# Optimization experiments

Hardware: AMD Instinct MI355X
Metric: run time of the kernel (lower is better)

## Reference

```python
import jax, jax.numpy as jnp
import numpy as np

N_NODES = 100000
N_EDGES = 3200000
D_FEAT = 256
GC_HID = 20      # CVAEEncoder.hidden_dim default
DEC_HID = 40     # CVAEDecoder.hidden_dim default
Z_DIM = 32
EXPR_DIM = 256
SIGMA_BOUND = 0.0001


def setup_inputs() -> dict:
    key = jax.random.key(0)
    ks = jax.random.split(key, 16)
    inp = {
        "nodes": jax.random.normal(ks[0], (N_NODES, D_FEAT), dtype=jnp.float32),
        "senders": jax.random.randint(ks[1], (N_EDGES,), 0, N_NODES, dtype=jnp.int32),
        "receivers": jax.random.randint(ks[2], (N_EDGES,), 0, N_NODES, dtype=jnp.int32),
        "eps": jax.random.normal(ks[3], (N_NODES, Z_DIM), dtype=jnp.float32),
    }
    def dense(k, fan_in, fan_out):
        # flax default: lecun_normal kernel, zero bias
        w = jax.random.normal(k, (fan_in, fan_out), dtype=jnp.float32) / np.sqrt(fan_in)
        return w, jnp.zeros((fan_out,), jnp.float32)
    inp["W_gc1"], inp["b_gc1"] = dense(ks[4], D_FEAT, GC_HID)
    inp["W_gc2"], inp["b_gc2"] = dense(ks[5], GC_HID, GC_HID)
    inp["W_mu"], inp["b_mu"] = dense(ks[6], GC_HID + D_FEAT, Z_DIM)
    inp["W_ls"], inp["b_ls"] = dense(ks[7], GC_HID + D_FEAT, Z_DIM)
    inp["W_d1"], inp["b_d1"] = dense(ks[8], Z_DIM, DEC_HID)
    inp["W_d2"], inp["b_d2"] = dense(ks[9], DEC_HID, EXPR_DIM)
    return inp


def _gcn_layer(h, senders, receivers, W, b):
    # jraph.GraphConvolution: update_node_fn = softmax(relu(Dense(x))),
    # then symmetric-normalized segment_sum aggregation (no self edges).
    h = jax.nn.softmax(jax.nn.relu(h @ W + b), axis=-1)  # [N, GC_HID]
    ones = jnp.ones(senders.shape, h.dtype)
    deg_s = jax.ops.segment_sum(ones, senders, N_NODES)
    deg_r = jax.ops.segment_sum(ones, receivers, N_NODES)
    h = h * jax.lax.rsqrt(jnp.maximum(deg_s, 1.0))[:, None]
    h = jax.ops.segment_sum(h[senders], receivers, N_NODES)  # irregular gather+scatter
    h = h * jax.lax.rsqrt(jnp.maximum(deg_r, 1.0))[:, None]
    return h


def reference(nodes, senders, receivers, eps,
              W_gc1, b_gc1, W_gc2, b_gc2,
              W_mu, b_mu, W_ls, b_ls,
              W_d1, b_d1, W_d2, b_d2):
    # Encoder: 2 GC layers
    h = _gcn_layer(nodes, senders, receivers, W_gc1, b_gc1)
    h = _gcn_layer(h, senders, receivers, W_gc2, b_gc2)
    h = jnp.concatenate([h, nodes], axis=-1)  # [N, GC_HID + D_FEAT]
    mu = h @ W_mu + b_mu
    logsig2 = h @ W_ls + b_ls
    # Reparameterization
    sigma = SIGMA_BOUND + jnp.exp(0.5 * logsig2)
    z = mu + sigma * eps
    # Decoder MLP (nlayers=2 -> one hidden relu layer)
    d = jax.nn.relu(z @ W_d1 + b_d1)
    Xsample = d @ W_d2 + b_d2
    return Xsample, mu, logsig2
```

## Files before the change

kernel.cpp:

```cpp
#include <hip/hip_runtime.h>
#include <math.h>

#define N_NODES 100000
#define N_EDGES 3200000
#define D_FEAT 256
#define GC_HID 20
#define DEC_HID 40
#define Z_DIM 32

#define EPB 2048
#define NBLK 1563
#define SB 392
#define SBSH 8
#define S2CAP 12288


__device__ inline unsigned short f2bf(float f) {
    unsigned u = __float_as_uint(f);
    return (unsigned short)((u + 0x7FFFu + ((u >> 16) & 1u)) >> 16);
}
__device__ inline float bf2f(unsigned short h) {
    return __uint_as_float((unsigned)h << 16);
}

__global__ __launch_bounds__(96) void k_wpack(const float* __restrict__ W1,
                                              const float* __restrict__ Wmu,
                                              const float* __restrict__ Wls,
                                              float* __restrict__ Wp) {
    int k = blockIdx.x, j = threadIdx.x;
    float v = 0.0f;
    if (j < 20) v = W1[k * GC_HID + j];
    else if (j >= 24 && j < 56) v = Wmu[(GC_HID + k) * Z_DIM + (j - 24)];
    else if (j >= 56 && j < 88) v = Wls[(GC_HID + k) * Z_DIM + (j - 56)];
    Wp[k * 96 + j] = v;
}

__global__ __launch_bounds__(512) void k_sort(const int* __restrict__ snd,
                                              const int* __restrict__ rcv,
                                              unsigned* __restrict__ rec_r,
                                              unsigned char* __restrict__ rec_s,
                                              unsigned short* __restrict__ srow_r,
                                              unsigned short* __restrict__ srow_s) {
    __shared__ int es[EPB], er[EPB];
    __shared__ unsigned scan[SB + 1];
    __shared__ unsigned cur[SB];
    __shared__ unsigned sorted[EPB];
    __shared__ unsigned char sorteds[EPB];
    int b = blockIdx.x, t = threadIdx.x;
    int base = b * EPB;
    int cnt = min(EPB, N_EDGES - base);
    for (int i = t; i < cnt; i += 512) { es[i] = snd[base + i]; er[i] = rcv[base + i]; }

    for (int i = t; i < SB + 1; i += 512) scan[i] = 0u;
    __syncthreads();
    for (int i = t; i < cnt; i += 512) atomicAdd(&scan[(er[i] >> SBSH) + 1], 1u);
    __syncthreads();
    for (int off = 1; off < SB + 1; off <<= 1) {
        unsigned v = (t >= off && t < SB + 1) ? scan[t - off] : 0u;
        __syncthreads();
        if (t < SB + 1) scan[t] += v;
        __syncthreads();
    }
    for (int i = t; i < SB + 1; i += 512) srow_r[(size_t)b * (SB + 1) + i] = (unsigned short)scan[i];
    if (t < SB) cur[t] = scan[t];
    __syncthreads();
    for (int i = t; i < cnt; i += 512) {
        int r = er[i];
        unsigned pos = atomicAdd(&cur[r >> SBSH], 1u);
        sorted[pos] = ((unsigned)(r & 255) << 17) | (unsigned)es[i];
    }
    __syncthreads();
    for (int i = t; i < cnt; i += 512) rec_r[(size_t)base + i] = sorted[i];
    __syncthreads();

    for (int i = t; i < SB + 1; i += 512) scan[i] = 0u;
    __syncthreads();
    for (int i = t; i < cnt; i += 512) atomicAdd(&scan[(es[i] >> SBSH) + 1], 1u);
    __syncthreads();
    for (int off = 1; off < SB + 1; off <<= 1) {
        unsigned v = (t >= off && t < SB + 1) ? scan[t - off] : 0u;
        __syncthreads();
        if (t < SB + 1) scan[t] += v;
        __syncthreads();
    }
    for (int i = t; i < SB + 1; i += 512) srow_s[(size_t)b * (SB + 1) + i] = (unsigned short)scan[i];
    if (t < SB) cur[t] = scan[t];
    __syncthreads();
    for (int i = t; i < cnt; i += 512) {
        int s = es[i];
        unsigned pos = atomicAdd(&cur[s >> SBSH], 1u);
        sorteds[pos] = (unsigned char)(s & 255);
    }
    __syncthreads();
    for (int i = t; i < cnt; i += 512) rec_s[(size_t)base + i] = sorteds[i];
}

__global__ __launch_bounds__(512) void k_degs(const unsigned char* __restrict__ rec_s,
                                              const unsigned short* __restrict__ srow_s,
                                              float* __restrict__ rs_s) {
    __shared__ unsigned h[256];
    int s = blockIdx.x, t = threadIdx.x;
    if (t < 256) h[t] = 0u;
    __syncthreads();
    for (int k = t; k < NBLK; k += 512) {
        const unsigned short* row = srow_s + (size_t)k * (SB + 1);
        unsigned st = row[s], en = row[s + 1];
        const unsigned char* rp = rec_s + (size_t)k * EPB;
        for (unsigned i = st; i < en; ++i) atomicAdd(&h[rp[i]], 1u);
    }
    __syncthreads();
    if (t < 256) {
        int n = (s << SBSH) + t;
        if (n < N_NODES) rs_s[n] = rsqrtf(fmaxf((float)h[t], 1.0f));
    }
}

__global__ __launch_bounds__(256) void k_scanB(const unsigned short* __restrict__ srow_r,
                                               unsigned* __restrict__ pref_t,
                                               unsigned* __restrict__ gtot) {
    __shared__ unsigned buf[256];
    int s = blockIdx.x, t = threadIdx.x;
    unsigned run = 0;
    for (int k0 = 0; k0 < NBLK; k0 += 256) {
        int k = k0 + t;
        unsigned v = 0;
        if (k < NBLK) {
            const unsigned short* row = srow_r + (size_t)k * (SB + 1);
            v = (unsigned)row[s + 1] - (unsigned)row[s];
        }
        buf[t] = v;
        __syncthreads();
        for (int off = 1; off < 256; off <<= 1) {
            unsigned x = (t >= off) ? buf[t - off] : 0u;
            __syncthreads();
            buf[t] += x;
            __syncthreads();
        }
        if (k < NBLK) pref_t[(size_t)s * NBLK + k] = run + (buf[t] - v);
        unsigned tot = buf[255];
        __syncthreads();
        run += tot;
    }
    if (t == 0) gtot[s] = run;
}

__global__ __launch_bounds__(512) void k_scanG(const unsigned* __restrict__ gtot,
                                               unsigned* __restrict__ gbase) {
    __shared__ unsigned buf[SB];
    int t = threadIdx.x;
    if (t < SB) buf[t] = gtot[t];
    __syncthreads();
    for (int off = 1; off < SB; off <<= 1) {
        unsigned x = (t >= off && t < SB) ? buf[t - off] : 0u;
        __syncthreads();
        if (t < SB) buf[t] += x;
        __syncthreads();
    }
    if (t < SB) gbase[t + 1] = buf[t];
    if (t == 0) gbase[0] = 0u;
}

__global__ __launch_bounds__(256) void k_gscat(const unsigned* __restrict__ rec_r,
                                               const unsigned short* __restrict__ srow_r,
                                               const unsigned* __restrict__ pref_t,
                                               const unsigned* __restrict__ gbase,
                                               unsigned* __restrict__ grec) {
    __shared__ unsigned recs[EPB];
    __shared__ unsigned short srow[SB + 1];
    int b = blockIdx.x, t = threadIdx.x;
    int base = b * EPB;
    int cnt = min(EPB, N_EDGES - base);
    for (int i = t; i < cnt; i += 256) recs[i] = rec_r[(size_t)base + i];
    for (int i = t; i < SB + 1; i += 256) srow[i] = srow_r[(size_t)b * (SB + 1) + i];
    __syncthreads();
    for (int s = t; s < SB; s += 256) {
        unsigned lo = srow[s], hi = srow[s + 1];
        if (lo == hi) continue;
        unsigned dst = gbase[s] + pref_t[(size_t)s * NBLK + b];
        for (unsigned i = lo; i < hi; ++i) grec[dst + (i - lo)] = recs[i];
    }
}

__global__ __launch_bounds__(256) void k_sort2(unsigned* __restrict__ grec,
                                               const unsigned* __restrict__ gbase,
                                               unsigned* __restrict__ row_ptr) {
    __shared__ unsigned recs[S2CAP];
    __shared__ unsigned hist[256];
    __shared__ unsigned scan[256];
    __shared__ unsigned cur[256];
    int s = blockIdx.x, t = threadIdx.x;
    unsigned lo = gbase[s], hi = gbase[s + 1];
    unsigned cnt = min(hi - lo, (unsigned)S2CAP);
    for (unsigned i = t; i < cnt; i += 256) recs[i] = grec[lo + i];
    hist[t] = 0u;
    __syncthreads();
    for (unsigned i = t; i < cnt; i += 256) atomicAdd(&hist[recs[i] >> 17], 1u);
    __syncthreads();
    unsigned v = hist[t];
    scan[t] = v;
    __syncthreads();
    for (int off = 1; off < 256; off <<= 1) {
        unsigned x = (t >= off) ? scan[t - off] : 0u;
        __syncthreads();
        scan[t] += x;
        __syncthreads();
    }
    unsigned excl = scan[t] - v;
    {
        int n = (s << SBSH) + t;
        if (n <= N_NODES) row_ptr[n] = lo + excl;
    }
    cur[t] = excl;
    __syncthreads();
    for (unsigned i = t; i < cnt; i += 256) {
        unsigned rec = recs[i];
        unsigned pos = atomicAdd(&cur[rec >> 17], 1u);
        grec[lo + pos] = rec & 0x1FFFFu;
    }
}

__global__ __launch_bounds__(320) void k_gather(const unsigned* __restrict__ row_ptr,
                                                const unsigned* __restrict__ grec,
                                                const float* __restrict__ src,
                                                float* __restrict__ dst) {
    int gid = blockIdx.x * 320 + threadIdx.x;
    int node = gid / 5, q = gid % 5;
    if (node >= N_NODES) return;
    unsigned lo = row_ptr[node], hi = row_ptr[node + 1];
    float4 a0 = make_float4(0.f, 0.f, 0.f, 0.f);
    float4 a1 = make_float4(0.f, 0.f, 0.f, 0.f);
    float4 a2 = make_float4(0.f, 0.f, 0.f, 0.f);
    float4 a3 = make_float4(0.f, 0.f, 0.f, 0.f);
    unsigned e = lo;
    for (; e + 4 <= hi; e += 4) {
        unsigned s0 = grec[e], s1 = grec[e + 1], s2 = grec[e + 2], s3 = grec[e + 3];
        float4 v0 = ((const float4*)src)[s0 * 5 + q];
        float4 v1 = ((const float4*)src)[s1 * 5 + q];
        float4 v2 = ((const float4*)src)[s2 * 5 + q];
        float4 v3 = ((const float4*)src)[s3 * 5 + q];
        a0.x += v0.x; a0.y += v0.y; a0.z += v0.z; a0.w += v0.w;
        a1.x += v1.x; a1.y += v1.y; a1.z += v1.z; a1.w += v1.w;
        a2.x += v2.x; a2.y += v2.y; a2.z += v2.z; a2.w += v2.w;
        a3.x += v3.x; a3.y += v3.y; a3.z += v3.z; a3.w += v3.w;
    }
    for (; e < hi; ++e) {
        unsigned s0 = grec[e];
        float4 v0 = ((const float4*)src)[s0 * 5 + q];
        a0.x += v0.x; a0.y += v0.y; a0.z += v0.z; a0.w += v0.w;
    }
    a0.x += a1.x + a2.x + a3.x;
    a0.y += a1.y + a2.y + a3.y;
    a0.z += a1.z + a2.z + a3.z;
    a0.w += a1.w + a2.w + a3.w;
    float sc = rsqrtf(fmaxf((float)(hi - lo), 1.0f));
    a0.x *= sc; a0.y *= sc; a0.z *= sc; a0.w *= sc;
    ((float4*)dst)[node * 5 + q] = a0;
}

__global__ __launch_bounds__(320) void k_gg1(const unsigned* __restrict__ row_ptr,
                                             const unsigned* __restrict__ grec,
                                             const float* __restrict__ src,
                                             const float* __restrict__ W2,
                                             const float* __restrict__ b2,
                                             const float* __restrict__ rs_s,
                                             float* __restrict__ h2_pre) {
    __shared__ float h1[64 * 21];
    __shared__ float Wsh[GC_HID * GC_HID];
    __shared__ float bsh[GC_HID];
    int t = threadIdx.x;
    if (t < GC_HID * GC_HID) Wsh[t] = W2[t];
    if (t >= 400 && t < 400 + GC_HID) bsh[t - 400] = b2[t - 400];
    int nl = t / 5, q = t % 5;
    int node = blockIdx.x * 64 + nl;
    bool live = (node < N_NODES);
    unsigned lo = 0, hi = 0;
    if (live) { lo = row_ptr[node]; hi = row_ptr[node + 1]; }
    float4 a0 = make_float4(0.f, 0.f, 0.f, 0.f);
    float4 a1 = make_float4(0.f, 0.f, 0.f, 0.f);
    float4 a2 = make_float4(0.f, 0.f, 0.f, 0.f);
    float4 a3 = make_float4(0.f, 0.f, 0.f, 0.f);
    unsigned e = lo;
    for (; e + 4 <= hi; e += 4) {
        unsigned s0 = grec[e], s1 = grec[e + 1], s2 = grec[e + 2], s3 = grec[e + 3];
        float4 v0 = ((const float4*)src)[s0 * 5 + q];
        float4 v1 = ((const float4*)src)[s1 * 5 + q];
        float4 v2 = ((const float4*)src)[s2 * 5 + q];
        float4 v3 = ((const float4*)src)[s3 * 5 + q];
        a0.x += v0.x; a0.y += v0.y; a0.z += v0.z; a0.w += v0.w;
        a1.x += v1.x; a1.y += v1.y; a1.z += v1.z; a1.w += v1.w;
        a2.x += v2.x; a2.y += v2.y; a2.z += v2.z; a2.w += v2.w;
        a3.x += v3.x; a3.y += v3.y; a3.z += v3.z; a3.w += v3.w;
    }
    for (; e < hi; ++e) {
        unsigned s0 = grec[e];
        float4 v0 = ((const float4*)src)[s0 * 5 + q];
        a0.x += v0.x; a0.y += v0.y; a0.z += v0.z; a0.w += v0.w;
    }
    a0.x += a1.x + a2.x + a3.x;
    a0.y += a1.y + a2.y + a3.y;
    a0.z += a1.z + a2.z + a3.z;
    a0.w += a1.w + a2.w + a3.w;
    if (live) {
        float sc = rsqrtf(fmaxf((float)(hi - lo), 1.0f));
        float* row = &h1[nl * 21 + q * 4];
        row[0] = a0.x * sc; row[1] = a0.y * sc;
        row[2] = a0.z * sc; row[3] = a0.w * sc;
    }
    __syncthreads();
    if (t < 64) {
        int nn = blockIdx.x * 64 + t;
        if (nn < N_NODES) {
            float hv[GC_HID];
#pragma unroll
            for (int i = 0; i < GC_HID; ++i) hv[i] = h1[t * 21 + i];
            float o[GC_HID];
#pragma unroll
            for (int j = 0; j < GC_HID; ++j) o[j] = bsh[j];
#pragma unroll
            for (int i = 0; i < GC_HID; ++i) {
                float x = hv[i];
#pragma unroll
                for (int j = 0; j < GC_HID; ++j) o[j] = fmaf(x, Wsh[i * GC_HID + j], o[j]);
            }
            float mx = -1e30f;
#pragma unroll
            for (int j = 0; j < GC_HID; ++j) { o[j] = fmaxf(o[j], 0.0f); mx = fmaxf(mx, o[j]); }
            float s = 0.0f;
#pragma unroll
            for (int j = 0; j < GC_HID; ++j) { o[j] = __expf(o[j] - mx); s += o[j]; }
            float inv = rs_s[nn] / s;
#pragma unroll
            for (int j = 0; j < GC_HID; ++j) o[j] *= inv;
            float4* op = (float4*)&h2_pre[(size_t)nn * GC_HID];
            op[0] = make_float4(o[0],  o[1],  o[2],  o[3]);
            op[1] = make_float4(o[4],  o[5],  o[6],  o[7]);
            op[2] = make_float4(o[8],  o[9],  o[10], o[11]);
            op[3] = make_float4(o[12], o[13], o[14], o[15]);
            op[4] = make_float4(o[16], o[17], o[18], o[19]);
        }
    }
}

__global__ __launch_bounds__(256) void k_gc1f(const float* __restrict__ nodes,
                                              const float* __restrict__ Wp,
                                              const float* __restrict__ b1,
                                              const float* __restrict__ rs_s,
                                              float* __restrict__ h_pre,
                                              unsigned short* __restrict__ pml) {
    __shared__ float tile[2][64 * 33];
    float* gb = &tile[0][0];
    int t = threadIdx.x;
    int g = __builtin_amdgcn_readfirstlane(t >> 6);
    int lane = t & 63;
    int n0 = blockIdx.x * 64;
    int node = n0 + lane;

    {
        int idx = t;
#pragma unroll
        for (int r = 0; r < 2; ++r, idx += 256) {
            int rr = idx >> 3, c4 = idx & 7;
            int gn = n0 + rr;
            float4 v = (gn < N_NODES)
                ? ((const float4*)nodes)[(size_t)gn * 64 + c4]
                : make_float4(0.f, 0.f, 0.f, 0.f);
            float* dst = &tile[0][rr * 33 + c4 * 4];
            dst[0] = v.x; dst[1] = v.y; dst[2] = v.z; dst[3] = v.w;
        }
    }
    __syncthreads();

    float acc[24];
#pragma unroll
    for (int j = 0; j < 24; ++j) acc[j] = 0.0f;

    for (int c = 0; c < 8; ++c) {
        float4 p0, p1;
        if (c < 7) {
            int idx = t, rr = idx >> 3, c4 = idx & 7, gn = n0 + rr;
            p0 = (gn < N_NODES)
                ? ((const float4*)nodes)[(size_t)gn * 64 + (c + 1) * 8 + c4]
                : make_float4(0.f, 0.f, 0.f, 0.f);
            idx = t + 256; rr = idx >> 3; c4 = idx & 7; gn = n0 + rr;
            p1 = (gn < N_NODES)
                ? ((const float4*)nodes)[(size_t)gn * 64 + (c + 1) * 8 + c4]
                : make_float4(0.f, 0.f, 0.f, 0.f);
        }
        const float* trow  = &tile[c & 1][lane * 33];
        const float* wbase = Wp + (size_t)(c * 32) * 96 + g * 24;
#pragma unroll 4
        for (int kk = 0; kk < 32; ++kk) {
            float x = trow[kk];
            const float* wr = wbase + kk * 96;
#pragma unroll
            for (int j = 0; j < 24; ++j) acc[j] = fmaf(x, wr[j], acc[j]);
        }
        if (c < 7) {
            int idx = t, rr = idx >> 3, c4 = idx & 7;
            float* dst = &tile[(c + 1) & 1][rr * 33 + c4 * 4];
            dst[0] = p0.x; dst[1] = p0.y; dst[2] = p0.z; dst[3] = p0.w;
            idx = t + 256; rr = idx >> 3; c4 = idx & 7;
            dst = &tile[(c + 1) & 1][rr * 33 + c4 * 4];
            dst[0] = p1.x; dst[1] = p1.y; dst[2] = p1.z; dst[3] = p1.w;
        }
        __syncthreads();
    }

    if (node < N_NODES) {
        if (g == 0) {
#pragma unroll
            for (int j = 0; j < GC_HID; ++j) gb[lane * 21 + j] = acc[j] + b1[j];
        } else {
            int base = (g - 1) * 24;
            unsigned short* pp = pml + (size_t)node * 64 + base;
            uint4 q0, q1, q2;
            q0.x = (unsigned)f2bf(acc[0]) | ((unsigned)f2bf(acc[1]) << 16);
            q0.y = (unsigned)f2bf(acc[2]) | ((unsigned)f2bf(acc[3]) << 16);
            q0.z = (unsigned)f2bf(acc[4]) | ((unsigned)f2bf(acc[5]) << 16);
            q0.w = (unsigned)f2bf(acc[6]) | ((unsigned)f2bf(acc[7]) << 16);
            q1.x = (unsigned)f2bf(acc[8]) | ((unsigned)f2bf(acc[9]) << 16);
            q1.y = (unsigned)f2bf(acc[10]) | ((unsigned)f2bf(acc[11]) << 16);
            q1.z = (unsigned)f2bf(acc[12]) | ((unsigned)f2bf(acc[13]) << 16);
            q1.w = (unsigned)f2bf(acc[14]) | ((unsigned)f2bf(acc[15]) << 16);
            q2.x = (unsigned)f2bf(acc[16]) | ((unsigned)f2bf(acc[17]) << 16);
            q2.y = (unsigned)f2bf(acc[18]) | ((unsigned)f2bf(acc[19]) << 16);
            q2.z = (unsigned)f2bf(acc[20]) | ((unsigned)f2bf(acc[21]) << 16);
            q2.w = (unsigned)f2bf(acc[22]) | ((unsigned)f2bf(acc[23]) << 16);
            ((uint4*)pp)[0] = q0;
            ((uint4*)pp)[1] = q1;
            if (g != 3) ((uint4*)pp)[2] = q2;
        }
    }
    __syncthreads();
    if (t < 64) {
        int nn = n0 + t;
        if (nn < N_NODES) {
            float v[GC_HID];
            float mx = -1e30f;
#pragma unroll
            for (int j = 0; j < GC_HID; ++j) {
                v[j] = fmaxf(gb[t * 21 + j], 0.0f);
                mx = fmaxf(mx, v[j]);
            }
            float s = 0.0f;
#pragma unroll
            for (int j = 0; j < GC_HID; ++j) {
                v[j] = __expf(v[j] - mx);
                s += v[j];
            }
            float inv = rs_s[nn] / s;
#pragma unroll
            for (int j = 0; j < GC_HID; ++j) v[j] *= inv;
            float4* o = (float4*)&h_pre[(size_t)nn * GC_HID];
            o[0] = make_float4(v[0],  v[1],  v[2],  v[3]);
            o[1] = make_float4(v[4],  v[5],  v[6],  v[7]);
            o[2] = make_float4(v[8],  v[9],  v[10], v[11]);
            o[3] = make_float4(v[12], v[13], v[14], v[15]);
            o[4] = make_float4(v[16], v[17], v[18], v[19]);
        }
    }
}

__global__ __launch_bounds__(256) void k_enc2(const float* __restrict__ h2in,
                                              const unsigned short* __restrict__ pml,
                                              const float* __restrict__ Wmu,
                                              const float* __restrict__ bmu,
                                              const float* __restrict__ Wls,
                                              const float* __restrict__ bls,
                                              float* __restrict__ mu_out,
                                              float* __restrict__ ls_out) {
    int t = threadIdx.x;
    int wave = t >> 6, lane = t & 63;
    int og = __builtin_amdgcn_readfirstlane(wave | ((int)blockIdx.y << 2));
    int half = og >> 2;
    int co = (og & 3) << 3;
    int node = blockIdx.x * 64 + lane;
    if (node >= N_NODES) return;
    const float* W  = half ? Wls : Wmu;
    const float* bb = half ? bls : bmu;
    float* out      = half ? ls_out : mu_out;

    uint4 p = *(const uint4*)(pml + (size_t)node * 64 + half * 32 + co);
    float acc[8];
    acc[0] = bf2f((unsigned short)(p.x & 0xFFFFu));
    acc[1] = bf2f((unsigned short)(p.x >> 16));
    acc[2] = bf2f((unsigned short)(p.y & 0xFFFFu));
    acc[3] = bf2f((unsigned short)(p.y >> 16));
    acc[4] = bf2f((unsigned short)(p.z & 0xFFFFu));
    acc[5] = bf2f((unsigned short)(p.z >> 16));
    acc[6] = bf2f((unsigned short)(p.w & 0xFFFFu));
    acc[7] = bf2f((unsigned short)(p.w >> 16));
#pragma unroll
    for (int j = 0; j < 8; ++j) acc[j] += bb[co + j];

    const float4* hp = (const float4*)(h2in + (size_t)node * GC_HID);
#pragma unroll
    for (int v = 0; v < 5; ++v) {
        float4 hh = hp[v];
#pragma unroll
        for (int c = 0; c < 4; ++c) {
            float x = (c == 0) ? hh.x : (c == 1) ? hh.y : (c == 2) ? hh.z : hh.w;
            const float* wr = W + (v * 4 + c) * Z_DIM + co;
#pragma unroll
            for (int j = 0; j < 8; ++j) acc[j] = fmaf(x, wr[j], acc[j]);
        }
    }
    float4* op = (float4*)(out + (size_t)node * Z_DIM + co);
    op[0] = make_float4(acc[0], acc[1], acc[2], acc[3]);
    op[1] = make_float4(acc[4], acc[5], acc[6], acc[7]);
}

__global__ __launch_bounds__(256) void k_decd(const float* __restrict__ mu,
                                              const float* __restrict__ ls,
                                              const float* __restrict__ eps,
                                              const float* __restrict__ Wd1,
                                              const float* __restrict__ bd1,
                                              float* __restrict__ dbuf) {
    int node = blockIdx.x * 256 + threadIdx.x;
    if (node >= N_NODES) return;
    float d[DEC_HID];
#pragma unroll
    for (int j = 0; j < DEC_HID; ++j) d[j] = bd1[j];
    const float4* mp = (const float4*)(mu + (size_t)node * Z_DIM);
    const float4* lp = (const float4*)(ls + (size_t)node * Z_DIM);
    const float4* ep = (const float4*)(eps + (size_t)node * Z_DIM);
#pragma unroll
    for (int v = 0; v < Z_DIM / 4; ++v) {
        float4 m = mp[v], l = lp[v], e = ep[v];
        float4 zz;
        zz.x = m.x + (1e-4f + __expf(0.5f * l.x)) * e.x;
        zz.y = m.y + (1e-4f + __expf(0.5f * l.y)) * e.y;
        zz.z = m.z + (1e-4f + __expf(0.5f * l.z)) * e.z;
        zz.w = m.w + (1e-4f + __expf(0.5f * l.w)) * e.w;
#pragma unroll
        for (int c = 0; c < 4; ++c) {
            float x = (c == 0) ? zz.x : (c == 1) ? zz.y : (c == 2) ? zz.z : zz.w;
            const float* wr = Wd1 + (v * 4 + c) * DEC_HID;
#pragma unroll
            for (int j = 0; j < DEC_HID; ++j) d[j] = fmaf(x, wr[j], d[j]);
        }
    }
    float4* op = (float4*)(dbuf + (size_t)node * DEC_HID);
#pragma unroll
    for (int v = 0; v < DEC_HID / 4; ++v)
        op[v] = make_float4(fmaxf(d[4*v], 0.f), fmaxf(d[4*v+1], 0.f),
                            fmaxf(d[4*v+2], 0.f), fmaxf(d[4*v+3], 0.f));
}

__global__ __launch_bounds__(256) void k_decx(const float* __restrict__ dbuf,
                                              const float* __restrict__ Wd2,
                                              const float* __restrict__ bd2,
                                              float* __restrict__ X) {
    int lane = threadIdx.x & 63;
    int wv   = threadIdx.x >> 6;
    int ch   = __builtin_amdgcn_readfirstlane(((blockIdx.x & 1) << 2) | wv);
    int node = (blockIdx.x >> 1) * 64 + lane;
    if (node >= N_NODES) return;
    int co = ch << 5;
    float o[32];
#pragma unroll
    for (int j = 0; j < 32; ++j) o[j] = bd2[co + j];
    const float4* dp = (const float4*)(dbuf + (size_t)node * DEC_HID);
#pragma unroll
    for (int v = 0; v < DEC_HID / 4; ++v) {
        float4 dd = dp[v];
#pragma unroll
        for (int c = 0; c < 4; ++c) {
            float x = (c == 0) ? dd.x : (c == 1) ? dd.y : (c == 2) ? dd.z : dd.w;
            const float* wr = Wd2 + (v * 4 + c) * D_FEAT + co;
#pragma unroll
            for (int j = 0; j < 32; ++j) o[j] = fmaf(x, wr[j], o[j]);
        }
    }
    float4* xp = (float4*)(X + (size_t)node * D_FEAT + co);
#pragma unroll
    for (int v = 0; v < 8; ++v)
        xp[v] = make_float4(o[4*v], o[4*v+1], o[4*v+2], o[4*v+3]);
}

extern "C" void kernel_launch(void* const* d_in, const int* in_sizes, int n_in,
                              void* d_out, int out_size, void* d_ws, size_t ws_size,
                              hipStream_t stream) {
    const float* nodes = (const float*)d_in[0];
    const int*   snd   = (const int*)d_in[1];
    const int*   rcv   = (const int*)d_in[2];
    const float* eps   = (const float*)d_in[3];
    const float* W1    = (const float*)d_in[4];
    const float* b1    = (const float*)d_in[5];
    const float* W2    = (const float*)d_in[6];
    const float* b2    = (const float*)d_in[7];
    const float* Wmu   = (const float*)d_in[8];
    const float* bmu   = (const float*)d_in[9];
    const float* Wls   = (const float*)d_in[10];
    const float* bls   = (const float*)d_in[11];
    const float* Wd1   = (const float*)d_in[12];
    const float* bd1   = (const float*)d_in[13];
    const float* Wd2   = (const float*)d_in[14];
    const float* bd2   = (const float*)d_in[15];

    char* ws = (char*)d_ws;
    float*          h_pre    = (float*)(ws);
    float*          agg      = (float*)(ws + 8000000);
    float*          dbuf     = (float*)(ws);
    unsigned*       grec     = (unsigned*)(ws + 16000000);
    unsigned*       rec_r    = (unsigned*)(ws + 28804096);
    unsigned short* pml      = (unsigned short*)(ws + 28804096);
    unsigned short* srow_r   = (unsigned short*)(ws + 41608192);
    unsigned*       pref_t   = (unsigned*)(ws + 42836720);
    unsigned*       row_ptr  = (unsigned*)(ws + 45287504);
    unsigned*       gtot     = (unsigned*)(ws + 45687508);
    unsigned*       gbase    = (unsigned*)(ws + 45689076);
    float*          rs_s     = (float*)(ws + 45690648);
    unsigned char*  rec_s    = (unsigned char*)(ws + 46090648);
    unsigned short* srow_s   = (unsigned short*)(ws + 49291672);
    float*          Wpack    = (float*)(ws + 50520192);

    float* X      = (float*)d_out;
    float* mu_out = X + (size_t)N_NODES * D_FEAT;
    float* ls_out = mu_out + (size_t)N_NODES * Z_DIM;

    k_wpack<<<256, 96, 0, stream>>>(W1, Wmu, Wls, Wpack);
    k_sort<<<NBLK, 512, 0, stream>>>(snd, rcv, rec_r, rec_s, srow_r, srow_s);
    k_degs<<<SB, 512, 0, stream>>>(rec_s, srow_s, rs_s);
    k_scanB<<<SB, 256, 0, stream>>>(srow_r, pref_t, gtot);
    k_scanG<<<1, 512, 0, stream>>>(gtot, gbase);
    k_gscat<<<NBLK, 256, 0, stream>>>(rec_r, srow_r, pref_t, gbase, grec);
    k_sort2<<<SB, 256, 0, stream>>>(grec, gbase, row_ptr);

    k_gc1f<<<1563, 256, 0, stream>>>(nodes, Wpack, b1, rs_s, h_pre, pml);
    k_gg1<<<1563, 320, 0, stream>>>(row_ptr, grec, h_pre, W2, b2, rs_s, agg);
    k_gather<<<1563, 320, 0, stream>>>(row_ptr, grec, agg, h_pre);

    k_enc2<<<dim3(1563, 2), 256, 0, stream>>>(h_pre, pml, Wmu, bmu, Wls, bls,
                                              mu_out, ls_out);
    k_decd<<<391, 256, 0, stream>>>(mu_out, ls_out, eps, Wd1, bd1, dbuf);
    k_decx<<<3126, 256, 0, stream>>>(dbuf, Wd2, bd2, X);
}
```

Measured before the change: 417.8 us.

## Fuse second gather with mu/logsig projection and merge decoder kernels

Merges the second-layer neighbor gather with the mu/logsig projection. The aggregated hidden vector goes to shared memory and is consumed straight away, so no h2 round-trip through global memory is needed. Also fuses the two decoder kernels into one, keeping the 40-wide hidden activation in shared memory instead of writing and re-reading dbuf. This removes launches and intermediate global traffic. In exchange, the gather phase leaves 192 of 512 threads idle, and the fused kernels have larger blocks, which may lower occupancy.

```diff
diff --git a/kernel.cpp b/kernel.cpp
--- a/kernel.cpp
+++ b/kernel.cpp
@@ -217,44 +217,6 @@
         unsigned pos = atomicAdd(&cur[rec >> 17], 1u);
         grec[lo + pos] = rec & 0x1FFFFu;
     }
-}
-
-__global__ __launch_bounds__(320) void k_gather(const unsigned* __restrict__ row_ptr,
-                                                const unsigned* __restrict__ grec,
-                                                const float* __restrict__ src,
-                                                float* __restrict__ dst) {
-    int gid = blockIdx.x * 320 + threadIdx.x;
-    int node = gid / 5, q = gid % 5;
-    if (node >= N_NODES) return;
-    unsigned lo = row_ptr[node], hi = row_ptr[node + 1];
-    float4 a0 = make_float4(0.f, 0.f, 0.f, 0.f);
-    float4 a1 = make_float4(0.f, 0.f, 0.f, 0.f);
-    float4 a2 = make_float4(0.f, 0.f, 0.f, 0.f);
-    float4 a3 = make_float4(0.f, 0.f, 0.f, 0.f);
-    unsigned e = lo;
-    for (; e + 4 <= hi; e += 4) {
-        unsigned s0 = grec[e], s1 = grec[e + 1], s2 = grec[e + 2], s3 = grec[e + 3];
-        float4 v0 = ((const float4*)src)[s0 * 5 + q];
-        float4 v1 = ((const float4*)src)[s1 * 5 + q];
-        float4 v2 = ((const float4*)src)[s2 * 5 + q];
-        float4 v3 = ((const float4*)src)[s3 * 5 + q];
-        a0.x += v0.x; a0.y += v0.y; a0.z += v0.z; a0.w += v0.w;
-        a1.x += v1.x; a1.y += v1.y; a1.z += v1.z; a1.w += v1.w;
-        a2.x += v2.x; a2.y += v2.y; a2.z += v2.z; a2.w += v2.w;
-        a3.x += v3.x; a3.y += v3.y; a3.z += v3.z; a3.w += v3.w;
-    }
-    for (; e < hi; ++e) {
-        unsigned s0 = grec[e];
-        float4 v0 = ((const float4*)src)[s0 * 5 + q];
-        a0.x += v0.x; a0.y += v0.y; a0.z += v0.z; a0.w += v0.w;
-    }
-    a0.x += a1.x + a2.x + a3.x;
-    a0.y += a1.y + a2.y + a3.y;
-    a0.z += a1.z + a2.z + a3.z;
-    a0.w += a1.w + a2.w + a3.w;
-    float sc = rsqrtf(fmaxf((float)(hi - lo), 1.0f));
-    a0.x *= sc; a0.y *= sc; a0.z *= sc; a0.w *= sc;
-    ((float4*)dst)[node * 5 + q] = a0;
 }
 
 __global__ __launch_bounds__(320) void k_gg1(const unsigned* __restrict__ row_ptr,
@@ -341,6 +303,93 @@
     }
 }
 
+__global__ __launch_bounds__(512) void k_gg2(const unsigned* __restrict__ row_ptr,
+                                             const unsigned* __restrict__ grec,
+                                             const float* __restrict__ src,
+                                             const unsigned short* __restrict__ pml,
+                                             const float* __restrict__ Wmu,
+                                             const float* __restrict__ bmu,
+                                             const float* __restrict__ Wls,
+                                             const float* __restrict__ bls,
+                                             float* __restrict__ mu_out,
+                                             float* __restrict__ ls_out) {
+    __shared__ float h2s[64 * 21];
+    int t = threadIdx.x;
+    int n0 = blockIdx.x * 64;
+    if (t < 320) {
+        int nl = t / 5, q = t % 5;
+        int node = n0 + nl;
+        bool live = (node < N_NODES);
+        unsigned lo = 0, hi = 0;
+        if (live) { lo = row_ptr[node]; hi = row_ptr[node + 1]; }
+        float4 a0 = make_float4(0.f, 0.f, 0.f, 0.f);
+        float4 a1 = make_float4(0.f, 0.f, 0.f, 0.f);
+        float4 a2 = make_float4(0.f, 0.f, 0.f, 0.f);
+        float4 a3 = make_float4(0.f, 0.f, 0.f, 0.f);
+        unsigned e = lo;
+        for (; e + 4 <= hi; e += 4) {
+            unsigned s0 = grec[e], s1 = grec[e + 1], s2 = grec[e + 2], s3 = grec[e + 3];
+            float4 v0 = ((const float4*)src)[s0 * 5 + q];
+            float4 v1 = ((const float4*)src)[s1 * 5 + q];
+            float4 v2 = ((const float4*)src)[s2 * 5 + q];
+            float4 v3 = ((const float4*)src)[s3 * 5 + q];
+            a0.x += v0.x; a0.y += v0.y; a0.z += v0.z; a0.w += v0.w;
+            a1.x += v1.x; a1.y += v1.y; a1.z += v1.z; a1.w += v1.w;
+            a2.x += v2.x; a2.y += v2.y; a2.z += v2.z; a2.w += v2.w;
+            a3.x += v3.x; a3.y += v3.y; a3.z += v3.z; a3.w += v3.w;
+        }
+        for (; e < hi; ++e) {
+            unsigned s0 = grec[e];
+            float4 v0 = ((const float4*)src)[s0 * 5 + q];
+            a0.x += v0.x; a0.y += v0.y; a0.z += v0.z; a0.w += v0.w;
+        }
+        a0.x += a1.x + a2.x + a3.x;
+        a0.y += a1.y + a2.y + a3.y;
+        a0.z += a1.z + a2.z + a3.z;
+        a0.w += a1.w + a2.w + a3.w;
+        if (live) {
+            float sc = rsqrtf(fmaxf((float)(hi - lo), 1.0f));
+            float* row = &h2s[nl * 21 + q * 4];
+            row[0] = a0.x * sc; row[1] = a0.y * sc;
+            row[2] = a0.z * sc; row[3] = a0.w * sc;
+        }
+    }
+    __syncthreads();
+    int wave = t >> 6, lane = t & 63;
+    int og = __builtin_amdgcn_readfirstlane(wave);
+    int half = og >> 2;
+    int co = (og & 3) << 3;
+    int node = n0 + lane;
+    if (node >= N_NODES) return;
+    const float* W  = half ? Wls : Wmu;
+    const float* bb = half ? bls : bmu;
+    float* out      = half ? ls_out : mu_out;
+
+    uint4 p = *(const uint4*)(pml + (size_t)node * 64 + half * 32 + co);
+    float acc[8];
+    acc[0] = bf2f((unsigned short)(p.x & 0xFFFFu));
+    acc[1] = bf2f((unsigned short)(p.x >> 16));
+    acc[2] = bf2f((unsigned short)(p.y & 0xFFFFu));
+    acc[3] = bf2f((unsigned short)(p.y >> 16));
+    acc[4] = bf2f((unsigned short)(p.z & 0xFFFFu));
+    acc[5] = bf2f((unsigned short)(p.z >> 16));
+    acc[6] = bf2f((unsigned short)(p.w & 0xFFFFu));
+    acc[7] = bf2f((unsigned short)(p.w >> 16));
+#pragma unroll
+    for (int j = 0; j < 8; ++j) acc[j] += bb[co + j];
+
+#pragma unroll
+    for (int i = 0; i < GC_HID; ++i) {
+        float x = h2s[lane * 21 + i];
+        const float* wr = W + i * Z_DIM + co;
+#pragma unroll
+        for (int j = 0; j < 8; ++j) acc[j] = fmaf(x, wr[j], acc[j]);
+    }
+    float4* op = (float4*)(out + (size_t)node * Z_DIM + co);
+    op[0] = make_float4(acc[0], acc[1], acc[2], acc[3]);
+    op[1] = make_float4(acc[4], acc[5], acc[6], acc[7]);
+}
+
 __global__ __launch_bounds__(256) void k_gc1f(const float* __restrict__ nodes,
                                               const float* __restrict__ Wp,
                                               const float* __restrict__ b1,
@@ -461,121 +510,77 @@
     }
 }
 
-__global__ __launch_bounds__(256) void k_enc2(const float* __restrict__ h2in,
-                                              const unsigned short* __restrict__ pml,
-                                              const float* __restrict__ Wmu,
-                                              const float* __restrict__ bmu,
-                                              const float* __restrict__ Wls,
-                                              const float* __restrict__ bls,
-                                              float* __restrict__ mu_out,
-                                              float* __restrict__ ls_out) {
+__global__ __launch_bounds__(512) void k_dec(const float* __restrict__ mu,
+                                             const float* __restrict__ ls,
+                                             const float* __restrict__ eps,
+                                             const float* __restrict__ Wd1,
+                                             const float* __restrict__ bd1,
+                                             const float* __restrict__ Wd2,
+                                             const float* __restrict__ bd2,
+                                             float* __restrict__ X) {
+    __shared__ float ds[128 * 41];
     int t = threadIdx.x;
     int wave = t >> 6, lane = t & 63;
-    int og = __builtin_amdgcn_readfirstlane(wave | ((int)blockIdx.y << 2));
-    int half = og >> 2;
-    int co = (og & 3) << 3;
-    int node = blockIdx.x * 64 + lane;
-    if (node >= N_NODES) return;
-    const float* W  = half ? Wls : Wmu;
-    const float* bb = half ? bls : bmu;
-    float* out      = half ? ls_out : mu_out;
-
-    uint4 p = *(const uint4*)(pml + (size_t)node * 64 + half * 32 + co);
-    float acc[8];
-    acc[0] = bf2f((unsigned short)(p.x & 0xFFFFu));
-    acc[1] = bf2f((unsigned short)(p.x >> 16));
-    acc[2] = bf2f((unsigned short)(p.y & 0xFFFFu));
-    acc[3] = bf2f((unsigned short)(p.y >> 16));
-    acc[4] = bf2f((unsigned short)(p.z & 0xFFFFu));
-    acc[5] = bf2f((unsigned short)(p.z >> 16));
-    acc[6] = bf2f((unsigned short)(p.w & 0xFFFFu));
-    acc[7] = bf2f((unsigned short)(p.w >> 16));
-#pragma unroll
-    for (int j = 0; j < 8; ++j) acc[j] += bb[co + j];
-
-    const float4* hp = (const float4*)(h2in + (size_t)node * GC_HID);
-#pragma unroll
-    for (int v = 0; v < 5; ++v) {
-        float4 hh = hp[v];
-#pragma unroll
-        for (int c = 0; c < 4; ++c) {
-            float x = (c == 0) ? hh.x : (c == 1) ? hh.y : (c == 2) ? hh.z : hh.w;
-            const float* wr = W + (v * 4 + c) * Z_DIM + co;
-#pragma unroll
-            for (int j = 0; j < 8; ++j) acc[j] = fmaf(x, wr[j], acc[j]);
-        }
-    }
-    float4* op = (float4*)(out + (size_t)node * Z_DIM + co);
-    op[0] = make_float4(acc[0], acc[1], acc[2], acc[3]);
-    op[1] = make_float4(acc[4], acc[5], acc[6], acc[7]);
-}
-
-__global__ __launch_bounds__(256) void k_decd(const float* __restrict__ mu,
-                                              const float* __restrict__ ls,
-                                              const float* __restrict__ eps,
-                                              const float* __restrict__ Wd1,
-                                              const float* __restrict__ bd1,
-                                              float* __restrict__ dbuf) {
-    int node = blockIdx.x * 256 + threadIdx.x;
-    if (node >= N_NODES) return;
-    float d[DEC_HID];
-#pragma unroll
-    for (int j = 0; j < DEC_HID; ++j) d[j] = bd1[j];
-    const float4* mp = (const float4*)(mu + (size_t)node * Z_DIM);
-    const float4* lp = (const float4*)(ls + (size_t)node * Z_DIM);
-    const float4* ep = (const float4*)(eps + (size_t)node * Z_DIM);
-#pragma unroll
-    for (int v = 0; v < Z_DIM / 4; ++v) {
-        float4 m = mp[v], l = lp[v], e = ep[v];
-        float4 zz;
-        zz.x = m.x + (1e-4f + __expf(0.5f * l.x)) * e.x;
-        zz.y = m.y + (1e-4f + __expf(0.5f * l.y)) * e.y;
-        zz.z = m.z + (1e-4f + __expf(0.5f * l.z)) * e.z;
-        zz.w = m.w + (1e-4f + __expf(0.5f * l.w)) * e.w;
-#pragma unroll
-        for (int c = 0; c < 4; ++c) {
-            float x = (c == 0) ? zz.x : (c == 1) ? zz.y : (c == 2) ? zz.z : zz.w;
-            const float* wr = Wd1 + (v * 4 + c) * DEC_HID;
-#pragma unroll
-            for (int j = 0; j < DEC_HID; ++j) d[j] = fmaf(x, wr[j], d[j]);
-        }
-    }
-    float4* op = (float4*)(dbuf + (size_t)node * DEC_HID);
-#pragma unroll
-    for (int v = 0; v < DEC_HID / 4; ++v)
-        op[v] = make_float4(fmaxf(d[4*v], 0.f), fmaxf(d[4*v+1], 0.f),
-                            fmaxf(d[4*v+2], 0.f), fmaxf(d[4*v+3], 0.f));
-}
-
-__global__ __launch_bounds__(256) void k_decx(const float* __restrict__ dbuf,
-                                              const float* __restrict__ Wd2,
-                                              const float* __restrict__ bd2,
-                                              float* __restrict__ X) {
-    int lane = threadIdx.x & 63;
-    int wv   = threadIdx.x >> 6;
-    int ch   = __builtin_amdgcn_readfirstlane(((blockIdx.x & 1) << 2) | wv);
-    int node = (blockIdx.x >> 1) * 64 + lane;
-    if (node >= N_NODES) return;
-    int co = ch << 5;
-    float o[32];
-#pragma unroll
-    for (int j = 0; j < 32; ++j) o[j] = bd2[co + j];
-    const float4* dp = (const float4*)(dbuf + (size_t)node * DEC_HID);
-#pragma unroll
-    for (int v = 0; v < DEC_HID / 4; ++v) {
-        float4 dd = dp[v];
-#pragma unroll
-        for (int c = 0; c < 4; ++c) {
-            float x = (c == 0) ? dd.x : (c == 1) ? dd.y : (c == 2) ? dd.z : dd.w;
-            const float* wr = Wd2 + (v * 4 + c) * D_FEAT + co;
-#pragma unroll
-            for (int j = 0; j < 32; ++j) o[j] = fmaf(x, wr[j], o[j]);
-        }
-    }
-    float4* xp = (float4*)(X + (size_t)node * D_FEAT + co);
-#pragma unroll
-    for (int v = 0; v < 8; ++v)
-        xp[v] = make_float4(o[4*v], o[4*v+1], o[4*v+2], o[4*v+3]);
+    int n0 = blockIdx.x * 128;
+    {
+        int wu = __builtin_amdgcn_readfirstlane(wave);
+        int qd = wu & 3;
+        int nh = wu >> 2;
+        int nrow = nh * 64 + lane;
+        int node = n0 + nrow;
+        if (node < N_NODES) {
+            float z[Z_DIM];
+            const float4* mp = (const float4*)(mu + (size_t)node * Z_DIM);
+            const float4* lp = (const float4*)(ls + (size_t)node * Z_DIM);
+            const float4* ep = (const float4*)(eps + (size_t)node * Z_DIM);
+#pragma unroll
+            for (int v = 0; v < Z_DIM / 4; ++v) {
+                float4 m = mp[v], l = lp[v], e = ep[v];
+                z[4*v+0] = m.x + (1e-4f + __expf(0.5f * l.x)) * e.x;
+                z[4*v+1] = m.y + (1e-4f + __expf(0.5f * l.y)) * e.y;
+                z[4*v+2] = m.z + (1e-4f + __expf(0.5f * l.z)) * e.z;
+                z[4*v+3] = m.w + (1e-4f + __expf(0.5f * l.w)) * e.w;
+            }
+            float d[10];
+#pragma unroll
+            for (int j = 0; j < 10; ++j) d[j] = bd1[qd * 10 + j];
+#pragma unroll
+            for (int i = 0; i < Z_DIM; ++i) {
+                float x = z[i];
+                const float* wr = Wd1 + i * DEC_HID + qd * 10;
+#pragma unroll
+                for (int j = 0; j < 10; ++j) d[j] = fmaf(x, wr[j], d[j]);
+            }
+            float* dst = &ds[nrow * 41 + qd * 10];
+#pragma unroll
+            for (int j = 0; j < 10; ++j) dst[j] = fmaxf(d[j], 0.0f);
+        }
+    }
+    __syncthreads();
+#pragma unroll
+    for (int p = 0; p < 2; ++p) {
+        int ch = __builtin_amdgcn_readfirstlane(wave >> 1) + p * 4;
+        int nrow = (wave & 1) * 64 + lane;
+        int node = n0 + nrow;
+        if (node < N_NODES) {
+            int co = ch << 5;
+            float o[32];
+#pragma unroll
+            for (int j = 0; j < 32; ++j) o[j] = bd2[co + j];
+            const float* drow = &ds[nrow * 41];
+#pragma unroll 8
+            for (int k = 0; k < DEC_HID; ++k) {
+                float x = drow[k];
+                const float* wr = Wd2 + k * D_FEAT + co;
+#pragma unroll
+                for (int j = 0; j < 32; ++j) o[j] = fmaf(x, wr[j], o[j]);
+            }
+            float4* xp = (float4*)(X + (size_t)node * D_FEAT + co);
+#pragma unroll
+            for (int v = 0; v < 8; ++v)
+                xp[v] = make_float4(o[4*v], o[4*v+1], o[4*v+2], o[4*v+3]);
+        }
+    }
 }
 
 extern "C" void kernel_launch(void* const* d_in, const int* in_sizes, int n_in,
@@ -601,7 +606,6 @@
     char* ws = (char*)d_ws;
     float*          h_pre    = (float*)(ws);
     float*          agg      = (float*)(ws + 8000000);
-    float*          dbuf     = (float*)(ws);
     unsigned*       grec     = (unsigned*)(ws + 16000000);
     unsigned*       rec_r    = (unsigned*)(ws + 28804096);
     unsigned short* pml      = (unsigned short*)(ws + 28804096);
@@ -629,10 +633,7 @@
 
     k_gc1f<<<1563, 256, 0, stream>>>(nodes, Wpack, b1, rs_s, h_pre, pml);
     k_gg1<<<1563, 320, 0, stream>>>(row_ptr, grec, h_pre, W2, b2, rs_s, agg);
-    k_gather<<<1563, 320, 0, stream>>>(row_ptr, grec, agg, h_pre);
-
-    k_enc2<<<dim3(1563, 2), 256, 0, stream>>>(h_pre, pml, Wmu, bmu, Wls, bls,
-                                              mu_out, ls_out);
-    k_decd<<<391, 256, 0, stream>>>(mu_out, ls_out, eps, Wd1, bd1, dbuf);
-    k_decx<<<3126, 256, 0, stream>>>(dbuf, Wd2, bd2, X);
-}
+    k_gg2<<<1563, 512, 0, stream>>>(row_ptr, grec, agg, pml, Wmu, bmu, Wls, bls,
+                                    mu_out, ls_out);
+    k_dec<<<782, 512, 0, stream>>>(mu_out, ls_out, eps, Wd1, bd1, Wd2, bd2, X);
+}
```

New measurement: 403.9 us. 3.3% less time.
